# Kernel optimization log

Measured on AMD Instinct MI355X. Metric: run time of the kernel, lower is better.

The kernel has to match this reference:

```python
import jax, jax.numpy as jnp
import numpy as np

R, C, B, E, H = 128, 256, 1, 768, 12
DK = E // H

def setup_inputs() -> dict:
    key = jax.random.key(0)
    ks = jax.random.split(key, 5)
    s = 1.0 / np.sqrt(E)
    return {
        "x": jax.random.normal(ks[0], (R, C, B, E), jnp.float32),
        "Wq": jax.random.normal(ks[1], (E, E), jnp.float32) * s,
        "bq": jnp.zeros((E,), jnp.float32),
        "Wk": jax.random.normal(ks[2], (E, E), jnp.float32) * s,
        "bk": jnp.zeros((E,), jnp.float32),
        "Wv": jax.random.normal(ks[3], (E, E), jnp.float32) * s,
        "bv": jnp.zeros((E,), jnp.float32),
        "Wo": jax.random.normal(ks[4], (E, E), jnp.float32) * s,
        "bo": jnp.zeros((E,), jnp.float32),
    }

def reference(x, Wq, bq, Wk, bk, Wv, bv, Wo, bo):
    n_rows, n_cols, batch, emb = x.shape
    scaling = (DK ** -0.5) / jnp.sqrt(jnp.float32(n_rows))
    # projections (torch Linear: x @ W.T + b)
    q = (x @ Wq.T + bq).reshape(n_rows, n_cols, batch, H, DK) * scaling
    k = (x @ Wk.T + bk).reshape(n_rows, n_cols, batch, H, DK)
    v = (x @ Wv.T + bv).reshape(n_rows, n_cols, batch, H, DK)
    # pooled attention logits: sum over rows r -> [H, B, C, C]
    attn = jnp.einsum('rinhd,rjnhd->hnij', q, k)
    probs = jax.nn.softmax(attn, axis=-1)  # single softmax shared across rows
    # context: [R, C, B, H, DK]
    c = jnp.einsum('hnij,rjnhd->rinhd', probs, v).reshape(n_rows, n_cols, batch, emb)
    out = c @ Wo.T + bo
    return out, probs
```

## Files before the change

kernel.cpp:

```cpp
#include <hip/hip_runtime.h>
#include <math.h>

#define R_  128
#define C_  256
#define E_  768
#define H_  12
#define DK_ 64
#define T_  (R_*C_)
#define RS_ 8
#define LP  40

typedef __attribute__((ext_vector_type(8))) short          bf16x8;
typedef __attribute__((ext_vector_type(4))) float          f32x4;
typedef __attribute__((ext_vector_type(4))) unsigned short u16x4;
typedef __attribute__((ext_vector_type(8))) unsigned short u16x8;

struct HL { unsigned short h, l; };

__device__ __forceinline__ HL split2(float f) {
    HL o;
    unsigned int u = __float_as_uint(f);
    o.h = (unsigned short)(u >> 16);
    float r = f - __uint_as_float(u & 0xFFFF0000u);
    o.l = (unsigned short)(__float_as_uint(r) >> 16);
    return o;
}

template<int AMODE, int OMODE>
__global__ __launch_bounds__(256, 2) void gemm_kernel(
    const float* __restrict__ A32,
    const unsigned short* __restrict__ Ah, const unsigned short* __restrict__ Al,
    const float* __restrict__ B32, const float* __restrict__ bias, float scale,
    float* __restrict__ Y32, unsigned short* __restrict__ Yh, unsigned short* __restrict__ Yl)
{
    __shared__ __align__(16) unsigned short smem[20480];
    unsigned short* AsH = smem;
    unsigned short* AsL = smem + 5120;
    unsigned short* BsH = smem + 10240;
    unsigned short* BsL = smem + 15360;

    const int tid  = threadIdx.x;
    const int m0   = blockIdx.x * 128;
    const int n0   = blockIdx.y * 128;
    const int wave = tid >> 6, lane = tid & 63;
    const int wm   = (wave & 1) * 64, wn = (wave >> 1) * 64;
    const int fr   = lane & 15;
    const int kq   = (lane >> 4) * 8;
    const int srow = tid >> 1;
    const int sk   = (tid & 1) * 16;

    f32x4 acc[4][4] = {};

    for (int k0 = 0; k0 < E_; k0 += 32) {
        if constexpr (AMODE == 0) {
            const float* ap = A32 + (size_t)(m0 + srow) * E_ + k0 + sk;
            #pragma unroll
            for (int c = 0; c < 4; ++c) {
                float4 f = *(const float4*)(ap + 4 * c);
                u16x4 h4, l4;
                HL e0 = split2(f.x), e1 = split2(f.y), e2 = split2(f.z), e3 = split2(f.w);
                h4[0] = e0.h; h4[1] = e1.h; h4[2] = e2.h; h4[3] = e3.h;
                l4[0] = e0.l; l4[1] = e1.l; l4[2] = e2.l; l4[3] = e3.l;
                *(u16x4*)&AsH[srow * LP + sk + 4 * c] = h4;
                *(u16x4*)&AsL[srow * LP + sk + 4 * c] = l4;
            }
        } else {
            const unsigned short* aph = Ah + (size_t)(m0 + srow) * E_ + k0 + sk;
            const unsigned short* apl = Al + (size_t)(m0 + srow) * E_ + k0 + sk;
            *(u16x8*)&AsH[srow * LP + sk]     = *(const u16x8*)aph;
            *(u16x8*)&AsH[srow * LP + sk + 8] = *(const u16x8*)(aph + 8);
            *(u16x8*)&AsL[srow * LP + sk]     = *(const u16x8*)apl;
            *(u16x8*)&AsL[srow * LP + sk + 8] = *(const u16x8*)(apl + 8);
        }
        {
            const float* bp = B32 + (size_t)(n0 + srow) * E_ + k0 + sk;
            #pragma unroll
            for (int c = 0; c < 4; ++c) {
                float4 f = *(const float4*)(bp + 4 * c);
                u16x4 h4, l4;
                HL e0 = split2(f.x), e1 = split2(f.y), e2 = split2(f.z), e3 = split2(f.w);
                h4[0] = e0.h; h4[1] = e1.h; h4[2] = e2.h; h4[3] = e3.h;
                l4[0] = e0.l; l4[1] = e1.l; l4[2] = e2.l; l4[3] = e3.l;
                *(u16x4*)&BsH[srow * LP + sk + 4 * c] = h4;
                *(u16x4*)&BsL[srow * LP + sk + 4 * c] = l4;
            }
        }
        __syncthreads();

        bf16x8 a_h[4], a_l[4], b_h[4], b_l[4];
        #pragma unroll
        for (int t = 0; t < 4; ++t) {
            a_h[t] = *(const bf16x8*)&AsH[(wm + t * 16 + fr) * LP + kq];
            a_l[t] = *(const bf16x8*)&AsL[(wm + t * 16 + fr) * LP + kq];
            b_h[t] = *(const bf16x8*)&BsH[(wn + t * 16 + fr) * LP + kq];
            b_l[t] = *(const bf16x8*)&BsL[(wn + t * 16 + fr) * LP + kq];
        }
        #pragma unroll
        for (int i = 0; i < 4; ++i)
            #pragma unroll
            for (int j = 0; j < 4; ++j) {
                acc[i][j] = __builtin_amdgcn_mfma_f32_16x16x32_bf16(a_h[i], b_h[j], acc[i][j], 0, 0, 0);
                acc[i][j] = __builtin_amdgcn_mfma_f32_16x16x32_bf16(a_h[i], b_l[j], acc[i][j], 0, 0, 0);
                acc[i][j] = __builtin_amdgcn_mfma_f32_16x16x32_bf16(a_l[i], b_h[j], acc[i][j], 0, 0, 0);
            }
        __syncthreads();
    }

    float* rep = (float*)smem + wave * 1024;
    const int mr = lane >> 2;
    const int nc = (lane & 3) * 16;
    #pragma unroll
    for (int ti = 0; ti < 4; ++ti) {
        __syncthreads();
        #pragma unroll
        for (int tj = 0; tj < 4; ++tj)
            #pragma unroll
            for (int r = 0; r < 4; ++r)
                rep[((lane >> 4) * 4 + r) * 64 + tj * 16 + fr] = acc[ti][tj][r];
        __syncthreads();
        float v[16];
        #pragma unroll
        for (int c = 0; c < 4; ++c)
            *(float4*)&v[4 * c] = *(const float4*)&rep[mr * 64 + nc + 4 * c];
        const int gm = m0 + wm + ti * 16 + mr;
        const int gn = n0 + wn + nc;
        if constexpr (OMODE == 1) {
            #pragma unroll
            for (int c = 0; c < 4; ++c) {
                float4 bv = *(const float4*)&bias[gn + 4 * c];
                float4 o;
                o.x = (v[4*c+0] + bv.x) * scale; o.y = (v[4*c+1] + bv.y) * scale;
                o.z = (v[4*c+2] + bv.z) * scale; o.w = (v[4*c+3] + bv.w) * scale;
                *(float4*)&Y32[(size_t)gm * E_ + gn + 4 * c] = o;
            }
        } else {
            unsigned short hh[16], ll[16];
            #pragma unroll
            for (int c = 0; c < 4; ++c) {
                float4 bv = *(const float4*)&bias[gn + 4 * c];
                HL e0 = split2((v[4*c+0] + bv.x) * scale);
                HL e1 = split2((v[4*c+1] + bv.y) * scale);
                HL e2 = split2((v[4*c+2] + bv.z) * scale);
                HL e3 = split2((v[4*c+3] + bv.w) * scale);
                hh[4*c+0] = e0.h; ll[4*c+0] = e0.l;
                hh[4*c+1] = e1.h; ll[4*c+1] = e1.l;
                hh[4*c+2] = e2.h; ll[4*c+2] = e2.l;
                hh[4*c+3] = e3.h; ll[4*c+3] = e3.l;
            }
            u16x8 H0, H1, L0, L1;
            #pragma unroll
            for (int j = 0; j < 8; ++j) { H0[j] = hh[j]; H1[j] = hh[8+j]; L0[j] = ll[j]; L1[j] = ll[8+j]; }
            *(u16x8*)&Yh[(size_t)gm * E_ + gn]     = H0;
            *(u16x8*)&Yh[(size_t)gm * E_ + gn + 8] = H1;
            *(u16x8*)&Yl[(size_t)gm * E_ + gn]     = L0;
            *(u16x8*)&Yl[(size_t)gm * E_ + gn + 8] = L1;
        }
    }
}

__global__ __launch_bounds__(256, 2) void attn_mfma(
    const unsigned short* __restrict__ Qh, const unsigned short* __restrict__ Ql,
    const unsigned short* __restrict__ Kh, const unsigned short* __restrict__ Kl,
    float* __restrict__ part)
{
    __shared__ __align__(16) unsigned short smem[20480];
    unsigned short* AsH = smem;
    unsigned short* AsL = smem + 5120;
    unsigned short* BsH = smem + 10240;
    unsigned short* BsL = smem + 15360;

    const int tid  = threadIdx.x;
    const int i0   = blockIdx.x * 128;
    const int j0   = blockIdx.y * 128;
    const int hz   = blockIdx.z;
    const int h    = hz >> 3;
    const int rc   = hz & 7;
    const int wave = tid >> 6, lane = tid & 63;
    const int wm   = (wave & 1) * 64, wn = (wave >> 1) * 64;
    const int fr   = lane & 15;
    const int kq   = (lane >> 4) * 8;
    const int srow = tid >> 1;
    const int sk   = (tid & 1) * 16;

    f32x4 acc[4][4] = {};

    for (int s = 0; s < 32; ++s) {
        const int r  = rc * 16 + (s >> 1);
        const int d0 = (s & 1) * 32;
        const size_t qb = ((size_t)(r * C_) + i0 + srow) * E_ + h * DK_ + d0 + sk;
        const size_t kb = ((size_t)(r * C_) + j0 + srow) * E_ + h * DK_ + d0 + sk;
        *(u16x8*)&AsH[srow * LP + sk]     = *(const u16x8*)&Qh[qb];
        *(u16x8*)&AsH[srow * LP + sk + 8] = *(const u16x8*)&Qh[qb + 8];
        *(u16x8*)&AsL[srow * LP + sk]     = *(const u16x8*)&Ql[qb];
        *(u16x8*)&AsL[srow * LP + sk + 8] = *(const u16x8*)&Ql[qb + 8];
        *(u16x8*)&BsH[srow * LP + sk]     = *(const u16x8*)&Kh[kb];
        *(u16x8*)&BsH[srow * LP + sk + 8] = *(const u16x8*)&Kh[kb + 8];
        *(u16x8*)&BsL[srow * LP + sk]     = *(const u16x8*)&Kl[kb];
        *(u16x8*)&BsL[srow * LP + sk + 8] = *(const u16x8*)&Kl[kb + 8];
        __syncthreads();

        bf16x8 a_h[4], a_l[4], b_h[4], b_l[4];
        #pragma unroll
        for (int t = 0; t < 4; ++t) {
            a_h[t] = *(const bf16x8*)&AsH[(wm + t * 16 + fr) * LP + kq];
            a_l[t] = *(const bf16x8*)&AsL[(wm + t * 16 + fr) * LP + kq];
            b_h[t] = *(const bf16x8*)&BsH[(wn + t * 16 + fr) * LP + kq];
            b_l[t] = *(const bf16x8*)&BsL[(wn + t * 16 + fr) * LP + kq];
        }
        #pragma unroll
        for (int i = 0; i < 4; ++i)
            #pragma unroll
            for (int j = 0; j < 4; ++j) {
                acc[i][j] = __builtin_amdgcn_mfma_f32_16x16x32_bf16(a_h[i], b_h[j], acc[i][j], 0, 0, 0);
                acc[i][j] = __builtin_amdgcn_mfma_f32_16x16x32_bf16(a_h[i], b_l[j], acc[i][j], 0, 0, 0);
                acc[i][j] = __builtin_amdgcn_mfma_f32_16x16x32_bf16(a_l[i], b_h[j], acc[i][j], 0, 0, 0);
            }
        __syncthreads();
    }

    float* rep = (float*)smem + wave * 1024;
    const int mr = lane >> 2;
    const int nc = (lane & 3) * 16;
    #pragma unroll
    for (int ti = 0; ti < 4; ++ti) {
        __syncthreads();
        #pragma unroll
        for (int tj = 0; tj < 4; ++tj)
            #pragma unroll
            for (int r = 0; r < 4; ++r)
                rep[((lane >> 4) * 4 + r) * 64 + tj * 16 + fr] = acc[ti][tj][r];
        __syncthreads();
        const int gi = i0 + wm + ti * 16 + mr;
        const int gj = j0 + wn + nc;
        #pragma unroll
        for (int c = 0; c < 4; ++c) {
            float4 o = *(const float4*)&rep[mr * 64 + nc + 4 * c];
            *(float4*)&part[((size_t)(rc * H_ + h) * C_ + gi) * C_ + gj + 4 * c] = o;
        }
    }
}

__global__ __launch_bounds__(256) void softmax_split(
    const float* __restrict__ part, float* __restrict__ probs,
    unsigned short* __restrict__ ph, unsigned short* __restrict__ pl)
{
    const int row = blockIdx.x;
    const int j = threadIdx.x;
    const int wave = j >> 6, lane = j & 63;

    float s = 0.0f;
    #pragma unroll
    for (int rcn = 0; rcn < RS_; ++rcn)
        s += part[((size_t)rcn * H_ * C_ + row) * C_ + j];

    float m = s;
    #pragma unroll
    for (int off = 32; off > 0; off >>= 1)
        m = fmaxf(m, __shfl_down(m, off, 64));
    __shared__ float redm[4];
    if (lane == 0) redm[wave] = m;
    __syncthreads();
    m = fmaxf(fmaxf(redm[0], redm[1]), fmaxf(redm[2], redm[3]));

    float e = expf(s - m);
    float t = e;
    #pragma unroll
    for (int off = 32; off > 0; off >>= 1)
        t += __shfl_down(t, off, 64);
    __shared__ float reds[4];
    if (lane == 0) reds[wave] = t;
    __syncthreads();
    t = reds[0] + reds[1] + reds[2] + reds[3];

    float p = e / t;
    probs[(size_t)row * C_ + j] = p;
    HL sp = split2(p);
    ph[(size_t)row * C_ + j] = sp.h;
    pl[(size_t)row * C_ + j] = sp.l;
}

__global__ __launch_bounds__(256, 2) void ctx_mfma(
    const unsigned short* __restrict__ Ph, const unsigned short* __restrict__ Pl,
    const unsigned short* __restrict__ Vh, const unsigned short* __restrict__ Vl,
    unsigned short* __restrict__ Ch, unsigned short* __restrict__ Cl)
{
    __shared__ __align__(16) unsigned short smem[15360];
    unsigned short* PsH = smem;
    unsigned short* PsL = smem + 5120;
    unsigned short* VsH = smem + 10240;
    unsigned short* VsL = smem + 12800;

    const int tid  = threadIdx.x;
    const int i0   = blockIdx.x * 128;
    const int r    = blockIdx.y;
    const int h    = blockIdx.z;
    const int wave = tid >> 6, lane = tid & 63;
    const int wm   = (wave & 1) * 64, wn = (wave >> 1) * 32;
    const int fr   = lane & 15;
    const int kq   = (lane >> 4) * 8;
    const int srow = tid >> 1;
    const int sk   = (tid & 1) * 16;
    const int vjj  = tid & 31;
    const int vdg  = tid >> 5;

    f32x4 acc[4][2] = {};

    for (int s = 0; s < 8; ++s) {
        const int jb = s * 32;
        const size_t pb = ((size_t)(h * C_) + i0 + srow) * C_ + jb + sk;
        *(u16x8*)&PsH[srow * LP + sk]     = *(const u16x8*)&Ph[pb];
        *(u16x8*)&PsH[srow * LP + sk + 8] = *(const u16x8*)&Ph[pb + 8];
        *(u16x8*)&PsL[srow * LP + sk]     = *(const u16x8*)&Pl[pb];
        *(u16x8*)&PsL[srow * LP + sk + 8] = *(const u16x8*)&Pl[pb + 8];
        const size_t vb = ((size_t)(r * C_) + jb + vjj) * E_ + h * DK_ + vdg * 8;
        u16x8 v_h = *(const u16x8*)&Vh[vb];
        u16x8 v_l = *(const u16x8*)&Vl[vb];
        #pragma unroll
        for (int u = 0; u < 8; ++u) {
            VsH[(vdg * 8 + u) * LP + vjj] = v_h[u];
            VsL[(vdg * 8 + u) * LP + vjj] = v_l[u];
        }
        __syncthreads();

        bf16x8 p_h[4], p_l[4], w_h[2], w_l[2];
        #pragma unroll
        for (int t = 0; t < 4; ++t) {
            p_h[t] = *(const bf16x8*)&PsH[(wm + t * 16 + fr) * LP + kq];
            p_l[t] = *(const bf16x8*)&PsL[(wm + t * 16 + fr) * LP + kq];
        }
        #pragma unroll
        for (int t = 0; t < 2; ++t) {
            w_h[t] = *(const bf16x8*)&VsH[(wn + t * 16 + fr) * LP + kq];
            w_l[t] = *(const bf16x8*)&VsL[(wn + t * 16 + fr) * LP + kq];
        }
        #pragma unroll
        for (int i = 0; i < 4; ++i)
            #pragma unroll
            for (int j = 0; j < 2; ++j) {
                acc[i][j] = __builtin_amdgcn_mfma_f32_16x16x32_bf16(p_h[i], w_h[j], acc[i][j], 0, 0, 0);
                acc[i][j] = __builtin_amdgcn_mfma_f32_16x16x32_bf16(p_h[i], w_l[j], acc[i][j], 0, 0, 0);
                acc[i][j] = __builtin_amdgcn_mfma_f32_16x16x32_bf16(p_l[i], w_h[j], acc[i][j], 0, 0, 0);
            }
        __syncthreads();
    }

    float* rep = (float*)smem + wave * 512;
    const int mr = lane >> 2;
    const int nc = (lane & 3) * 8;
    #pragma unroll
    for (int ti = 0; ti < 4; ++ti) {
        __syncthreads();
        #pragma unroll
        for (int tj = 0; tj < 2; ++tj)
            #pragma unroll
            for (int rr = 0; rr < 4; ++rr)
                rep[((lane >> 4) * 4 + rr) * 32 + tj * 16 + fr] = acc[ti][tj][rr];
        __syncthreads();
        float v[8];
        *(float4*)&v[0] = *(const float4*)&rep[mr * 32 + nc];
        *(float4*)&v[4] = *(const float4*)&rep[mr * 32 + nc + 4];
        const int gm = r * C_ + i0 + wm + ti * 16 + mr;
        const int gn = h * DK_ + wn + nc;
        u16x8 H8, L8;
        #pragma unroll
        for (int jj = 0; jj < 8; ++jj) { HL e = split2(v[jj]); H8[jj] = e.h; L8[jj] = e.l; }
        *(u16x8*)&Ch[(size_t)gm * E_ + gn] = H8;
        *(u16x8*)&Cl[(size_t)gm * E_ + gn] = L8;
    }
}

extern "C" void kernel_launch(void* const* d_in, const int* in_sizes, int n_in,
                              void* d_out, int out_size, void* d_ws, size_t ws_size,
                              hipStream_t stream)
{
    (void)in_sizes; (void)n_in; (void)out_size; (void)ws_size;

    const float* x  = (const float*)d_in[0];
    const float* Wq = (const float*)d_in[1];
    const float* bq = (const float*)d_in[2];
    const float* Wk = (const float*)d_in[3];
    const float* bk = (const float*)d_in[4];
    const float* Wv = (const float*)d_in[5];
    const float* bv = (const float*)d_in[6];
    const float* Wo = (const float*)d_in[7];
    const float* bo = (const float*)d_in[8];

    float* out   = (float*)d_out;
    float* probs = out + (size_t)T_ * E_;
    float* part  = out;

    const size_t QN = (size_t)T_ * E_;
    unsigned short* qh = (unsigned short*)d_ws;
    unsigned short* ql = qh + QN;
    unsigned short* kh = ql + QN;
    unsigned short* kl = kh + QN;
    unsigned short* vh = kl + QN;
    unsigned short* vl = vh + QN;
    unsigned short* ph = kh;
    unsigned short* pl = kh + (size_t)H_ * C_ * C_;
    unsigned short* ch = qh;
    unsigned short* cl = ql;

    const float scaling = 0.125f / sqrtf(128.0f);

    dim3 blk(256);
    gemm_kernel<0, 0><<<dim3(T_ / 128, E_ / 128), blk, 0, stream>>>(
        x, nullptr, nullptr, Wq, bq, scaling, nullptr, qh, ql);
    gemm_kernel<0, 0><<<dim3(T_ / 128, E_ / 128), blk, 0, stream>>>(
        x, nullptr, nullptr, Wk, bk, 1.0f, nullptr, kh, kl);
    gemm_kernel<0, 0><<<dim3(T_ / 128, E_ / 128), blk, 0, stream>>>(
        x, nullptr, nullptr, Wv, bv, 1.0f, nullptr, vh, vl);

    attn_mfma<<<dim3(C_ / 128, C_ / 128, H_ * RS_), blk, 0, stream>>>(qh, ql, kh, kl, part);
    softmax_split<<<dim3(H_ * C_), blk, 0, stream>>>(part, probs, ph, pl);
    ctx_mfma<<<dim3(C_ / 128, R_, H_), blk, 0, stream>>>(ph, pl, vh, vl, ch, cl);

    gemm_kernel<1, 1><<<dim3(T_ / 128, E_ / 128), blk, 0, stream>>>(
        nullptr, ch, cl, Wo, bo, 1.0f, out, nullptr, nullptr);
}
```

Measured before the change: 884.5 us.

## Fuse QKV GEMMs, widen GEMM tiles to 128x256, and rebalance attention split

The three Q/K/V projection GEMMs become one launch over a concatenated 2304-wide output, with the blockIdx order swapped so blocks sharing an x tile run together. All GEMMs use 128x256 tiles (8 accumulator columns per wave) to raise MFMA work per byte loaded into shared memory. The attention logit kernel now covers the full 256-column j range per block and splits rows into 32 chunks instead of 8, giving more blocks but more partial sums for softmax to reduce. The epilogue repack drops the inter-wave barriers in favour of per-wave padded scratch, at the cost of more registers and shared memory per block.

```diff
diff --git a/kernel.cpp b/kernel.cpp
--- a/kernel.cpp
+++ b/kernel.cpp
@@ -7,13 +7,15 @@
 #define H_  12
 #define DK_ 64
 #define T_  (R_*C_)
-#define RS_ 8
+#define RS_ 32
 #define LP  40
+#define REPP 132
 
 typedef __attribute__((ext_vector_type(8))) short          bf16x8;
 typedef __attribute__((ext_vector_type(4))) float          f32x4;
 typedef __attribute__((ext_vector_type(4))) unsigned short u16x4;
 typedef __attribute__((ext_vector_type(8))) unsigned short u16x8;
+typedef unsigned short ush;
 
 struct HL { unsigned short h, l; };
 
@@ -26,223 +28,197 @@
     return o;
 }
 
-template<int AMODE, int OMODE>
-__global__ __launch_bounds__(256, 2) void gemm_kernel(
-    const float* __restrict__ A32,
-    const unsigned short* __restrict__ Ah, const unsigned short* __restrict__ Al,
-    const float* __restrict__ B32, const float* __restrict__ bias, float scale,
-    float* __restrict__ Y32, unsigned short* __restrict__ Yh, unsigned short* __restrict__ Yl)
-{
-    __shared__ __align__(16) unsigned short smem[20480];
-    unsigned short* AsH = smem;
-    unsigned short* AsL = smem + 5120;
-    unsigned short* BsH = smem + 10240;
-    unsigned short* BsL = smem + 15360;
-
-    const int tid  = threadIdx.x;
-    const int m0   = blockIdx.x * 128;
-    const int n0   = blockIdx.y * 128;
+__device__ __forceinline__ void stage16_f32(ush* H, ush* L, int off, const float* src) {
+    #pragma unroll
+    for (int c = 0; c < 4; ++c) {
+        float4 f = *(const float4*)(src + 4 * c);
+        u16x4 h4, l4;
+        HL e0 = split2(f.x), e1 = split2(f.y), e2 = split2(f.z), e3 = split2(f.w);
+        h4[0] = e0.h; h4[1] = e1.h; h4[2] = e2.h; h4[3] = e3.h;
+        l4[0] = e0.l; l4[1] = e1.l; l4[2] = e2.l; l4[3] = e3.l;
+        *(u16x4*)&H[off + 4 * c] = h4;
+        *(u16x4*)&L[off + 4 * c] = l4;
+    }
+}
+
+__device__ __forceinline__ void stage16_pre(ush* H, ush* L, int off,
+                                            const ush* srcH, const ush* srcL) {
+    *(u16x8*)&H[off]     = *(const u16x8*)srcH;
+    *(u16x8*)&H[off + 8] = *(const u16x8*)(srcH + 8);
+    *(u16x8*)&L[off]     = *(const u16x8*)srcL;
+    *(u16x8*)&L[off + 8] = *(const u16x8*)(srcL + 8);
+}
+
+__device__ __forceinline__ void mma_step(
+    const ush* AsH, const ush* AsL, const ush* BsH, const ush* BsL,
+    int wm, int wn, int fr, int kq, f32x4 (&acc)[4][8])
+{
+    bf16x8 ah[4], al[4];
+    #pragma unroll
+    for (int t = 0; t < 4; ++t) {
+        ah[t] = *(const bf16x8*)&AsH[(wm + t * 16 + fr) * LP + kq];
+        al[t] = *(const bf16x8*)&AsL[(wm + t * 16 + fr) * LP + kq];
+    }
+    #pragma unroll
+    for (int j = 0; j < 8; ++j) {
+        bf16x8 bh = *(const bf16x8*)&BsH[(wn + j * 16 + fr) * LP + kq];
+        bf16x8 bl = *(const bf16x8*)&BsL[(wn + j * 16 + fr) * LP + kq];
+        #pragma unroll
+        for (int i = 0; i < 4; ++i) {
+            acc[i][j] = __builtin_amdgcn_mfma_f32_16x16x32_bf16(ah[i], bh, acc[i][j], 0, 0, 0);
+            acc[i][j] = __builtin_amdgcn_mfma_f32_16x16x32_bf16(ah[i], bl, acc[i][j], 0, 0, 0);
+            acc[i][j] = __builtin_amdgcn_mfma_f32_16x16x32_bf16(al[i], bh, acc[i][j], 0, 0, 0);
+        }
+    }
+}
+
+__device__ __forceinline__ void repack_ti(float* rep, const f32x4 (&arow)[8],
+                                          int lane, float (&v)[32])
+{
+    const int fr = lane & 15, q4 = lane >> 4;
+    #pragma unroll
+    for (int tj = 0; tj < 8; ++tj)
+        #pragma unroll
+        for (int r = 0; r < 4; ++r)
+            rep[(q4 * 4 + r) * REPP + tj * 16 + fr] = arow[tj][r];
+    asm volatile("" ::: "memory");
+    const int mr = lane >> 2, q = lane & 3;
+    #pragma unroll
+    for (int c = 0; c < 8; ++c)
+        *(float4*)&v[4 * c] = *(const float4*)&rep[mr * REPP + q * 32 + 4 * c];
+}
+
+__global__ __launch_bounds__(256, 2) void qkv_gemm(
+    const float* __restrict__ x,
+    const float* __restrict__ Wq, const float* __restrict__ bq,
+    const float* __restrict__ Wk, const float* __restrict__ bk,
+    const float* __restrict__ Wv, const float* __restrict__ bv,
+    float scaling,
+    ush* __restrict__ qh, ush* __restrict__ ql,
+    ush* __restrict__ kh, ush* __restrict__ kl,
+    ush* __restrict__ vh, ush* __restrict__ vl)
+{
+    __shared__ __align__(16) ush smem[30720];
+    ush* AsH = smem;
+    ush* AsL = smem + 5120;
+    ush* BsH = smem + 10240;
+    ush* BsL = smem + 20480;
+
+    const int n0g = blockIdx.x * 256;
+    const int m0  = blockIdx.y * 128;
+    const int mat = n0g / 768;
+    const int n0  = n0g - mat * 768;
+    const float* W    = (mat == 0) ? Wq : (mat == 1) ? Wk : Wv;
+    const float* bias = (mat == 0) ? bq : (mat == 1) ? bk : bv;
+    const float scale = (mat == 0) ? scaling : 1.0f;
+    ush* Yh = (mat == 0) ? qh : (mat == 1) ? kh : vh;
+    ush* Yl = (mat == 0) ? ql : (mat == 1) ? kl : vl;
+
+    const int tid = threadIdx.x;
     const int wave = tid >> 6, lane = tid & 63;
-    const int wm   = (wave & 1) * 64, wn = (wave >> 1) * 64;
-    const int fr   = lane & 15;
-    const int kq   = (lane >> 4) * 8;
-    const int srow = tid >> 1;
-    const int sk   = (tid & 1) * 16;
-
-    f32x4 acc[4][4] = {};
+    const int wm = (wave & 1) * 64, wn = (wave >> 1) * 128;
+    const int fr = lane & 15, kq = (lane >> 4) * 8;
+    const int arow = tid >> 1, koff = (tid & 1) * 16;
+
+    f32x4 acc[4][8] = {};
 
     for (int k0 = 0; k0 < E_; k0 += 32) {
-        if constexpr (AMODE == 0) {
-            const float* ap = A32 + (size_t)(m0 + srow) * E_ + k0 + sk;
+        stage16_f32(AsH, AsL, arow * LP + koff, x + (size_t)(m0 + arow) * E_ + k0 + koff);
+        #pragma unroll
+        for (int rr = 0; rr < 2; ++rr) {
+            const int brow = rr * 128 + arow;
+            stage16_f32(BsH, BsL, brow * LP + koff, W + (size_t)(n0 + brow) * E_ + k0 + koff);
+        }
+        __syncthreads();
+        mma_step(AsH, AsL, BsH, BsL, wm, wn, fr, kq, acc);
+        __syncthreads();
+    }
+
+    __syncthreads();
+    float* rep = (float*)smem + wave * (16 * REPP);
+    const int mr = lane >> 2, q = lane & 3;
+    #pragma unroll
+    for (int ti = 0; ti < 4; ++ti) {
+        float v[32];
+        repack_ti(rep, acc[ti], lane, v);
+        const int gm = m0 + wm + ti * 16 + mr;
+        const int gc = n0 + wn + q * 32;
+        #pragma unroll
+        for (int g = 0; g < 4; ++g) {
+            float4 b0 = *(const float4*)&bias[gc + 8 * g];
+            float4 b1 = *(const float4*)&bias[gc + 8 * g + 4];
+            float o[8] = {(v[8*g+0]+b0.x)*scale, (v[8*g+1]+b0.y)*scale,
+                          (v[8*g+2]+b0.z)*scale, (v[8*g+3]+b0.w)*scale,
+                          (v[8*g+4]+b1.x)*scale, (v[8*g+5]+b1.y)*scale,
+                          (v[8*g+6]+b1.z)*scale, (v[8*g+7]+b1.w)*scale};
+            u16x8 H8, L8;
             #pragma unroll
-            for (int c = 0; c < 4; ++c) {
-                float4 f = *(const float4*)(ap + 4 * c);
-                u16x4 h4, l4;
-                HL e0 = split2(f.x), e1 = split2(f.y), e2 = split2(f.z), e3 = split2(f.w);
-                h4[0] = e0.h; h4[1] = e1.h; h4[2] = e2.h; h4[3] = e3.h;
-                l4[0] = e0.l; l4[1] = e1.l; l4[2] = e2.l; l4[3] = e3.l;
-                *(u16x4*)&AsH[srow * LP + sk + 4 * c] = h4;
-                *(u16x4*)&AsL[srow * LP + sk + 4 * c] = l4;
-            }
-        } else {
-            const unsigned short* aph = Ah + (size_t)(m0 + srow) * E_ + k0 + sk;
-            const unsigned short* apl = Al + (size_t)(m0 + srow) * E_ + k0 + sk;
-            *(u16x8*)&AsH[srow * LP + sk]     = *(const u16x8*)aph;
-            *(u16x8*)&AsH[srow * LP + sk + 8] = *(const u16x8*)(aph + 8);
-            *(u16x8*)&AsL[srow * LP + sk]     = *(const u16x8*)apl;
-            *(u16x8*)&AsL[srow * LP + sk + 8] = *(const u16x8*)(apl + 8);
-        }
-        {
-            const float* bp = B32 + (size_t)(n0 + srow) * E_ + k0 + sk;
-            #pragma unroll
-            for (int c = 0; c < 4; ++c) {
-                float4 f = *(const float4*)(bp + 4 * c);
-                u16x4 h4, l4;
-                HL e0 = split2(f.x), e1 = split2(f.y), e2 = split2(f.z), e3 = split2(f.w);
-                h4[0] = e0.h; h4[1] = e1.h; h4[2] = e2.h; h4[3] = e3.h;
-                l4[0] = e0.l; l4[1] = e1.l; l4[2] = e2.l; l4[3] = e3.l;
-                *(u16x4*)&BsH[srow * LP + sk + 4 * c] = h4;
-                *(u16x4*)&BsL[srow * LP + sk + 4 * c] = l4;
-            }
-        }
-        __syncthreads();
-
-        bf16x8 a_h[4], a_l[4], b_h[4], b_l[4];
-        #pragma unroll
-        for (int t = 0; t < 4; ++t) {
-            a_h[t] = *(const bf16x8*)&AsH[(wm + t * 16 + fr) * LP + kq];
-            a_l[t] = *(const bf16x8*)&AsL[(wm + t * 16 + fr) * LP + kq];
-            b_h[t] = *(const bf16x8*)&BsH[(wn + t * 16 + fr) * LP + kq];
-            b_l[t] = *(const bf16x8*)&BsL[(wn + t * 16 + fr) * LP + kq];
-        }
-        #pragma unroll
-        for (int i = 0; i < 4; ++i)
-            #pragma unroll
-            for (int j = 0; j < 4; ++j) {
-                acc[i][j] = __builtin_amdgcn_mfma_f32_16x16x32_bf16(a_h[i], b_h[j], acc[i][j], 0, 0, 0);
-                acc[i][j] = __builtin_amdgcn_mfma_f32_16x16x32_bf16(a_h[i], b_l[j], acc[i][j], 0, 0, 0);
-                acc[i][j] = __builtin_amdgcn_mfma_f32_16x16x32_bf16(a_l[i], b_h[j], acc[i][j], 0, 0, 0);
-            }
-        __syncthreads();
-    }
-
-    float* rep = (float*)smem + wave * 1024;
-    const int mr = lane >> 2;
-    const int nc = (lane & 3) * 16;
+            for (int e = 0; e < 8; ++e) { HL s = split2(o[e]); H8[e] = s.h; L8[e] = s.l; }
+            *(u16x8*)&Yh[(size_t)gm * E_ + gc + 8 * g] = H8;
+            *(u16x8*)&Yl[(size_t)gm * E_ + gc + 8 * g] = L8;
+        }
+    }
+}
+
+__global__ __launch_bounds__(256, 2) void attn2(
+    const ush* __restrict__ Qh, const ush* __restrict__ Ql,
+    const ush* __restrict__ Kh, const ush* __restrict__ Kl,
+    float* __restrict__ part)
+{
+    __shared__ __align__(16) ush smem[30720];
+    ush* AsH = smem;
+    ush* AsL = smem + 5120;
+    ush* BsH = smem + 10240;
+    ush* BsL = smem + 20480;
+
+    const int i0 = blockIdx.x * 128;
+    const int z  = blockIdx.y;
+    const int h  = z >> 5;
+    const int rc = z & 31;
+
+    const int tid = threadIdx.x;
+    const int wave = tid >> 6, lane = tid & 63;
+    const int wm = (wave & 1) * 64, wn = (wave >> 1) * 128;
+    const int fr = lane & 15, kq = (lane >> 4) * 8;
+    const int arow = tid >> 1, koff = (tid & 1) * 16;
+
+    f32x4 acc[4][8] = {};
+
+    for (int s = 0; s < 8; ++s) {
+        const int r  = rc * 4 + (s >> 1);
+        const int d0 = (s & 1) * 32;
+        const size_t qb = ((size_t)(r * C_) + i0 + arow) * E_ + h * DK_ + d0 + koff;
+        stage16_pre(AsH, AsL, arow * LP + koff, Qh + qb, Ql + qb);
+        #pragma unroll
+        for (int rr = 0; rr < 2; ++rr) {
+            const int brow = rr * 128 + arow;
+            const size_t kb = ((size_t)(r * C_) + brow) * E_ + h * DK_ + d0 + koff;
+            stage16_pre(BsH, BsL, brow * LP + koff, Kh + kb, Kl + kb);
+        }
+        __syncthreads();
+        mma_step(AsH, AsL, BsH, BsL, wm, wn, fr, kq, acc);
+        __syncthreads();
+    }
+
+    __syncthreads();
+    float* rep = (float*)smem + wave * (16 * REPP);
+    const int mr = lane >> 2, q = lane & 3;
     #pragma unroll
     for (int ti = 0; ti < 4; ++ti) {
-        __syncthreads();
-        #pragma unroll
-        for (int tj = 0; tj < 4; ++tj)
-            #pragma unroll
-            for (int r = 0; r < 4; ++r)
-                rep[((lane >> 4) * 4 + r) * 64 + tj * 16 + fr] = acc[ti][tj][r];
-        __syncthreads();
-        float v[16];
-        #pragma unroll
-        for (int c = 0; c < 4; ++c)
-            *(float4*)&v[4 * c] = *(const float4*)&rep[mr * 64 + nc + 4 * c];
-        const int gm = m0 + wm + ti * 16 + mr;
-        const int gn = n0 + wn + nc;
-        if constexpr (OMODE == 1) {
-            #pragma unroll
-            for (int c = 0; c < 4; ++c) {
-                float4 bv = *(const float4*)&bias[gn + 4 * c];
-                float4 o;
-                o.x = (v[4*c+0] + bv.x) * scale; o.y = (v[4*c+1] + bv.y) * scale;
-                o.z = (v[4*c+2] + bv.z) * scale; o.w = (v[4*c+3] + bv.w) * scale;
-                *(float4*)&Y32[(size_t)gm * E_ + gn + 4 * c] = o;
-            }
-        } else {
-            unsigned short hh[16], ll[16];
-            #pragma unroll
-            for (int c = 0; c < 4; ++c) {
-                float4 bv = *(const float4*)&bias[gn + 4 * c];
-                HL e0 = split2((v[4*c+0] + bv.x) * scale);
-                HL e1 = split2((v[4*c+1] + bv.y) * scale);
-                HL e2 = split2((v[4*c+2] + bv.z) * scale);
-                HL e3 = split2((v[4*c+3] + bv.w) * scale);
-                hh[4*c+0] = e0.h; ll[4*c+0] = e0.l;
-                hh[4*c+1] = e1.h; ll[4*c+1] = e1.l;
-                hh[4*c+2] = e2.h; ll[4*c+2] = e2.l;
-                hh[4*c+3] = e3.h; ll[4*c+3] = e3.l;
-            }
-            u16x8 H0, H1, L0, L1;
-            #pragma unroll
-            for (int j = 0; j < 8; ++j) { H0[j] = hh[j]; H1[j] = hh[8+j]; L0[j] = ll[j]; L1[j] = ll[8+j]; }
-            *(u16x8*)&Yh[(size_t)gm * E_ + gn]     = H0;
-            *(u16x8*)&Yh[(size_t)gm * E_ + gn + 8] = H1;
-            *(u16x8*)&Yl[(size_t)gm * E_ + gn]     = L0;
-            *(u16x8*)&Yl[(size_t)gm * E_ + gn + 8] = L1;
-        }
-    }
-}
-
-__global__ __launch_bounds__(256, 2) void attn_mfma(
-    const unsigned short* __restrict__ Qh, const unsigned short* __restrict__ Ql,
-    const unsigned short* __restrict__ Kh, const unsigned short* __restrict__ Kl,
-    float* __restrict__ part)
-{
-    __shared__ __align__(16) unsigned short smem[20480];
-    unsigned short* AsH = smem;
-    unsigned short* AsL = smem + 5120;
-    unsigned short* BsH = smem + 10240;
-    unsigned short* BsL = smem + 15360;
-
-    const int tid  = threadIdx.x;
-    const int i0   = blockIdx.x * 128;
-    const int j0   = blockIdx.y * 128;
-    const int hz   = blockIdx.z;
-    const int h    = hz >> 3;
-    const int rc   = hz & 7;
-    const int wave = tid >> 6, lane = tid & 63;
-    const int wm   = (wave & 1) * 64, wn = (wave >> 1) * 64;
-    const int fr   = lane & 15;
-    const int kq   = (lane >> 4) * 8;
-    const int srow = tid >> 1;
-    const int sk   = (tid & 1) * 16;
-
-    f32x4 acc[4][4] = {};
-
-    for (int s = 0; s < 32; ++s) {
-        const int r  = rc * 16 + (s >> 1);
-        const int d0 = (s & 1) * 32;
-        const size_t qb = ((size_t)(r * C_) + i0 + srow) * E_ + h * DK_ + d0 + sk;
-        const size_t kb = ((size_t)(r * C_) + j0 + srow) * E_ + h * DK_ + d0 + sk;
-        *(u16x8*)&AsH[srow * LP + sk]     = *(const u16x8*)&Qh[qb];
-        *(u16x8*)&AsH[srow * LP + sk + 8] = *(const u16x8*)&Qh[qb + 8];
-        *(u16x8*)&AsL[srow * LP + sk]     = *(const u16x8*)&Ql[qb];
-        *(u16x8*)&AsL[srow * LP + sk + 8] = *(const u16x8*)&Ql[qb + 8];
-        *(u16x8*)&BsH[srow * LP + sk]     = *(const u16x8*)&Kh[kb];
-        *(u16x8*)&BsH[srow * LP + sk + 8] = *(const u16x8*)&Kh[kb + 8];
-        *(u16x8*)&BsL[srow * LP + sk]     = *(const u16x8*)&Kl[kb];
-        *(u16x8*)&BsL[srow * LP + sk + 8] = *(const u16x8*)&Kl[kb + 8];
-        __syncthreads();
-
-        bf16x8 a_h[4], a_l[4], b_h[4], b_l[4];
-        #pragma unroll
-        for (int t = 0; t < 4; ++t) {
-            a_h[t] = *(const bf16x8*)&AsH[(wm + t * 16 + fr) * LP + kq];
-            a_l[t] = *(const bf16x8*)&AsL[(wm + t * 16 + fr) * LP + kq];
-            b_h[t] = *(const bf16x8*)&BsH[(wn + t * 16 + fr) * LP + kq];
-            b_l[t] = *(const bf16x8*)&BsL[(wn + t * 16 + fr) * LP + kq];
-        }
-        #pragma unroll
-        for (int i = 0; i < 4; ++i)
-            #pragma unroll
-            for (int j = 0; j < 4; ++j) {
-                acc[i][j] = __builtin_amdgcn_mfma_f32_16x16x32_bf16(a_h[i], b_h[j], acc[i][j], 0, 0, 0);
-                acc[i][j] = __builtin_amdgcn_mfma_f32_16x16x32_bf16(a_h[i], b_l[j], acc[i][j], 0, 0, 0);
-                acc[i][j] = __builtin_amdgcn_mfma_f32_16x16x32_bf16(a_l[i], b_h[j], acc[i][j], 0, 0, 0);
-            }
-        __syncthreads();
-    }
-
-    float* rep = (float*)smem + wave * 1024;
-    const int mr = lane >> 2;
-    const int nc = (lane & 3) * 16;
-    #pragma unroll
-    for (int ti = 0; ti < 4; ++ti) {
-        __syncthreads();
-        #pragma unroll
-        for (int tj = 0; tj < 4; ++tj)
-            #pragma unroll
-            for (int r = 0; r < 4; ++r)
-                rep[((lane >> 4) * 4 + r) * 64 + tj * 16 + fr] = acc[ti][tj][r];
-        __syncthreads();
+        float v[32];
+        repack_ti(rep, acc[ti], lane, v);
         const int gi = i0 + wm + ti * 16 + mr;
-        const int gj = j0 + wn + nc;
-        #pragma unroll
-        for (int c = 0; c < 4; ++c) {
-            float4 o = *(const float4*)&rep[mr * 64 + nc + 4 * c];
-            *(float4*)&part[((size_t)(rc * H_ + h) * C_ + gi) * C_ + gj + 4 * c] = o;
-        }
+        const int gj = wn + q * 32;
+        float* dst = part + ((size_t)(rc * H_ + h) * C_ + gi) * C_ + gj;
+        #pragma unroll
+        for (int c = 0; c < 8; ++c)
+            *(float4*)&dst[4 * c] = *(const float4*)&v[4 * c];
     }
 }
 
 __global__ __launch_bounds__(256) void softmax_split(
     const float* __restrict__ part, float* __restrict__ probs,
-    unsigned short* __restrict__ ph, unsigned short* __restrict__ pl)
+    ush* __restrict__ ph, ush* __restrict__ pl)
 {
     const int row = blockIdx.x;
     const int j = threadIdx.x;
@@ -251,7 +227,7 @@
     float s = 0.0f;
     #pragma unroll
     for (int rcn = 0; rcn < RS_; ++rcn)
-        s += part[((size_t)rcn * H_ * C_ + row) * C_ + j];
+        s += part[(size_t)rcn * H_ * C_ * C_ + (size_t)row * C_ + j];
 
     float m = s;
     #pragma unroll
@@ -280,15 +256,15 @@
 }
 
 __global__ __launch_bounds__(256, 2) void ctx_mfma(
-    const unsigned short* __restrict__ Ph, const unsigned short* __restrict__ Pl,
-    const unsigned short* __restrict__ Vh, const unsigned short* __restrict__ Vl,
-    unsigned short* __restrict__ Ch, unsigned short* __restrict__ Cl)
-{
-    __shared__ __align__(16) unsigned short smem[15360];
-    unsigned short* PsH = smem;
-    unsigned short* PsL = smem + 5120;
-    unsigned short* VsH = smem + 10240;
-    unsigned short* VsL = smem + 12800;
+    const ush* __restrict__ Ph, const ush* __restrict__ Pl,
+    const ush* __restrict__ Vh, const ush* __restrict__ Vl,
+    ush* __restrict__ Ch, ush* __restrict__ Cl)
+{
+    __shared__ __align__(16) ush smem[15360];
+    ush* PsH = smem;
+    ush* PsL = smem + 5120;
+    ush* VsH = smem + 10240;
+    ush* VsL = smem + 12800;
 
     const int tid  = threadIdx.x;
     const int i0   = blockIdx.x * 128;
@@ -308,10 +284,7 @@
     for (int s = 0; s < 8; ++s) {
         const int jb = s * 32;
         const size_t pb = ((size_t)(h * C_) + i0 + srow) * C_ + jb + sk;
-        *(u16x8*)&PsH[srow * LP + sk]     = *(const u16x8*)&Ph[pb];
-        *(u16x8*)&PsH[srow * LP + sk + 8] = *(const u16x8*)&Ph[pb + 8];
-        *(u16x8*)&PsL[srow * LP + sk]     = *(const u16x8*)&Pl[pb];
-        *(u16x8*)&PsL[srow * LP + sk + 8] = *(const u16x8*)&Pl[pb + 8];
+        stage16_pre(PsH, PsL, srow * LP + sk, Ph + pb, Pl + pb);
         const size_t vb = ((size_t)(r * C_) + jb + vjj) * E_ + h * DK_ + vdg * 8;
         u16x8 v_h = *(const u16x8*)&Vh[vb];
         u16x8 v_l = *(const u16x8*)&Vl[vb];
@@ -366,6 +339,61 @@
         for (int jj = 0; jj < 8; ++jj) { HL e = split2(v[jj]); H8[jj] = e.h; L8[jj] = e.l; }
         *(u16x8*)&Ch[(size_t)gm * E_ + gn] = H8;
         *(u16x8*)&Cl[(size_t)gm * E_ + gn] = L8;
+    }
+}
+
+__global__ __launch_bounds__(256, 2) void oproj_gemm(
+    const ush* __restrict__ Ah, const ush* __restrict__ Al,
+    const float* __restrict__ W, const float* __restrict__ bias,
+    float* __restrict__ Y)
+{
+    __shared__ __align__(16) ush smem[30720];
+    ush* AsH = smem;
+    ush* AsL = smem + 5120;
+    ush* BsH = smem + 10240;
+    ush* BsL = smem + 20480;
+
+    const int n0 = blockIdx.x * 256;
+    const int m0 = blockIdx.y * 128;
+
+    const int tid = threadIdx.x;
+    const int wave = tid >> 6, lane = tid & 63;
+    const int wm = (wave & 1) * 64, wn = (wave >> 1) * 128;
+    const int fr = lane & 15, kq = (lane >> 4) * 8;
+    const int arow = tid >> 1, koff = (tid & 1) * 16;
+
+    f32x4 acc[4][8] = {};
+
+    for (int k0 = 0; k0 < E_; k0 += 32) {
+        const size_t ab = (size_t)(m0 + arow) * E_ + k0 + koff;
+        stage16_pre(AsH, AsL, arow * LP + koff, Ah + ab, Al + ab);
+        #pragma unroll
+        for (int rr = 0; rr < 2; ++rr) {
+            const int brow = rr * 128 + arow;
+            stage16_f32(BsH, BsL, brow * LP + koff, W + (size_t)(n0 + brow) * E_ + k0 + koff);
+        }
+        __syncthreads();
+        mma_step(AsH, AsL, BsH, BsL, wm, wn, fr, kq, acc);
+        __syncthreads();
+    }
+
+    __syncthreads();
+    float* rep = (float*)smem + wave * (16 * REPP);
+    const int mr = lane >> 2, q = lane & 3;
+    #pragma unroll
+    for (int ti = 0; ti < 4; ++ti) {
+        float v[32];
+        repack_ti(rep, acc[ti], lane, v);
+        const int gm = m0 + wm + ti * 16 + mr;
+        const int gc = n0 + wn + q * 32;
+        #pragma unroll
+        for (int c = 0; c < 8; ++c) {
+            float4 b4 = *(const float4*)&bias[gc + 4 * c];
+            float4 o;
+            o.x = v[4*c+0] + b4.x; o.y = v[4*c+1] + b4.y;
+            o.z = v[4*c+2] + b4.z; o.w = v[4*c+3] + b4.w;
+            *(float4*)&Y[(size_t)gm * E_ + gc + 4 * c] = o;
+        }
     }
 }
 
@@ -390,31 +418,27 @@
     float* part  = out;
 
     const size_t QN = (size_t)T_ * E_;
-    unsigned short* qh = (unsigned short*)d_ws;
-    unsigned short* ql = qh + QN;
-    unsigned short* kh = ql + QN;
-    unsigned short* kl = kh + QN;
-    unsigned short* vh = kl + QN;
-    unsigned short* vl = vh + QN;
-    unsigned short* ph = kh;
-    unsigned short* pl = kh + (size_t)H_ * C_ * C_;
-    unsigned short* ch = qh;
-    unsigned short* cl = ql;
+    ush* qh = (ush*)d_ws;
+    ush* ql = qh + QN;
+    ush* kh = ql + QN;
+    ush* kl = kh + QN;
+    ush* vh = kl + QN;
+    ush* vl = vh + QN;
+    ush* ph = kh;
+    ush* pl = kh + (size_t)H_ * C_ * C_;
+    ush* ch = qh;
+    ush* cl = ql;
 
     const float scaling = 0.125f / sqrtf(128.0f);
 
     dim3 blk(256);
-    gemm_kernel<0, 0><<<dim3(T_ / 128, E_ / 128), blk, 0, stream>>>(
-        x, nullptr, nullptr, Wq, bq, scaling, nullptr, qh, ql);
-    gemm_kernel<0, 0><<<dim3(T_ / 128, E_ / 128), blk, 0, stream>>>(
-        x, nullptr, nullptr, Wk, bk, 1.0f, nullptr, kh, kl);
-    gemm_kernel<0, 0><<<dim3(T_ / 128, E_ / 128), blk, 0, stream>>>(
-        x, nullptr, nullptr, Wv, bv, 1.0f, nullptr, vh, vl);
-
-    attn_mfma<<<dim3(C_ / 128, C_ / 128, H_ * RS_), blk, 0, stream>>>(qh, ql, kh, kl, part);
+    qkv_gemm<<<dim3(2304 / 256, T_ / 128), blk, 0, stream>>>(
+        x, Wq, bq, Wk, bk, Wv, bv, scaling, qh, ql, kh, kl, vh, vl);
+
+    attn2<<<dim3(C_ / 128, H_ * RS_), blk, 0, stream>>>(qh, ql, kh, kl, part);
+
     softmax_split<<<dim3(H_ * C_), blk, 0, stream>>>(part, probs, ph, pl);
+
     ctx_mfma<<<dim3(C_ / 128, R_, H_), blk, 0, stream>>>(ph, pl, vh, vl, ch, cl);
-
-    gemm_kernel<1, 1><<<dim3(T_ / 128, E_ / 128), blk, 0, stream>>>(
-        nullptr, ch, cl, Wo, bo, 1.0f, out, nullptr, nullptr);
-}
+    oproj_gemm<<<dim3(E_ / 256, T_ / 128), blk, 0, stream>>>(ch, cl, Wo, bo, out);
+}
```

Result: slower. 1.007 ms (+13.9%).
